# Kernel tuning notes

Hardware: AMD Instinct MI355X
Metric: run time of the kernel (lower is better)

The kernel has to match this reference:

```python
import jax, jax.numpy as jnp
import numpy as np

N, E = 50000, 800000
C = 64
L = 4
EPS_MSG = 1e-7  # GENConv message epsilon


def _bn(h, g, b):
    # BatchNorm over node dim (batch statistics)
    mu = h.mean(0)
    var = h.var(0)
    return (h - mu) * jax.lax.rsqrt(var + 1e-5) * g + b


def _ln(h, g, b):
    mu = h.mean(-1, keepdims=True)
    var = h.var(-1, keepdims=True)
    return (h - mu) * jax.lax.rsqrt(var + 1e-5) * g + b


def _enc(h, W1, b1, g1, B1, W2, b2):
    # PyG MLP(num_layers=2, norm=batch_norm, plain last layer); dropout=identity (eval)
    h = jax.nn.relu(_bn(h @ W1 + b1, g1, B1))
    return h @ W2 + b2


def _genconv(x, e, src, dst, W1, b1, g, B, W2, b2, t):
    n = x.shape[0]
    msg = jax.nn.relu(x[src] + e) + EPS_MSG            # [E, C]
    tm = t * msg
    mx = jax.ops.segment_max(tm, dst, num_segments=n)  # per-dst per-feature max
    w = jnp.exp(tm - mx[dst])
    denom = jax.ops.segment_sum(w, dst, num_segments=n)
    alpha = w / (denom[dst] + 1e-16)                   # scatter softmax weights
    aggr = jax.ops.segment_sum(msg * alpha, dst, num_segments=n)  # [N, C]
    h = aggr + x                                       # GENConv residual
    h = jax.nn.relu(_ln(h @ W1 + b1, g, B))            # inner MLP [C,2C,C]
    return h @ W2 + b2


def _forward(x, edge_attr, src, dst, nW1, nb1, ng1, nB1, nW2, nb2,
             eW1, eb1, eg1, eB1, eW2, eb2, lng, lnb,
             cW1, cb1, cg, cB, cW2, cb2, ct,
             oW1, ob1, og1, oB1, oW2, ob2, og2, oB2, oW3, ob3):
    h = _enc(x, nW1, nb1, ng1, nB1, nW2, nb2)          # [N, C]
    e = _enc(edge_attr, eW1, eb1, eg1, eB1, eW2, eb2)  # [E, C]
    # layers[0].conv applied directly (no pre-norm)
    h = _genconv(h, e, src, dst, cW1[0], cb1[0], cg[0], cB[0], cW2[0], cb2[0], ct[0])
    # DeepGCNLayer res+ : x + conv(relu(LN(x)))
    for l in range(1, L):
        r = jax.nn.relu(_ln(h, lng[l], lnb[l]))
        r = _genconv(r, e, src, dst, cW1[l], cb1[l], cg[l], cB[l], cW2[l], cb2[l], ct[l])
        h = h + r
    # out MLP [C, C//2, C//4, num_classes], batch_norm, plain last
    o = jax.nn.relu(_bn(h @ oW1 + ob1, og1, oB1))
    o = jax.nn.relu(_bn(o @ oW2 + ob2, og2, oB2))
    return o @ oW3 + ob3


def setup_inputs() -> dict:
    key = jax.random.key(0)
    ks = iter(jax.random.split(key, 32))
    def nrm(shape, s=0.05):
        return jax.random.normal(next(ks), shape, dtype=jnp.float32) * s
    inp = {}
    inp["x"] = nrm((N, 16), 1.0)
    inp["edge_attr"] = nrm((E, 8), 1.0)
    inp["edge_index"] = jax.random.randint(next(ks), (2, E), 0, N, dtype=jnp.int32)
    inp["nW1"] = nrm((16, C)); inp["nb1"] = jnp.zeros((C,)); inp["ng1"] = jnp.ones((C,)); inp["nB1"] = jnp.zeros((C,))
    inp["nW2"] = nrm((C, C)); inp["nb2"] = jnp.zeros((C,))
    inp["eW1"] = nrm((8, C)); inp["eb1"] = jnp.zeros((C,)); inp["eg1"] = jnp.ones((C,)); inp["eB1"] = jnp.zeros((C,))
    inp["eW2"] = nrm((C, C)); inp["eb2"] = jnp.zeros((C,))
    inp["lng"] = jnp.ones((L, C)); inp["lnb"] = jnp.zeros((L, C))
    inp["cW1"] = nrm((L, C, 2 * C)); inp["cb1"] = jnp.zeros((L, 2 * C))
    inp["cg"] = jnp.ones((L, 2 * C)); inp["cB"] = jnp.zeros((L, 2 * C))
    inp["cW2"] = nrm((L, 2 * C, C)); inp["cb2"] = jnp.zeros((L, C))
    inp["ct"] = jnp.ones((L,))
    inp["oW1"] = nrm((C, C // 2)); inp["ob1"] = jnp.zeros((C // 2,)); inp["og1"] = jnp.ones((C // 2,)); inp["oB1"] = jnp.zeros((C // 2,))
    inp["oW2"] = nrm((C // 2, C // 4)); inp["ob2"] = jnp.zeros((C // 4,)); inp["og2"] = jnp.ones((C // 4,)); inp["oB2"] = jnp.zeros((C // 4,))
    inp["oW3"] = nrm((C // 4, 2)); inp["ob3"] = jnp.zeros((2,))
    return inp


def reference(x, edge_attr, edge_index, nW1, nb1, ng1, nB1, nW2, nb2,
              eW1, eb1, eg1, eB1, eW2, eb2, lng, lnb,
              cW1, cb1, cg, cB, cW2, cb2, ct,
              oW1, ob1, og1, oB1, oW2, ob2, og2, oB2, oW3, ob3):
    src, dst = edge_index[0], edge_index[1]
    return _forward(x, edge_attr, src, dst, nW1, nb1, ng1, nB1, nW2, nb2,
                    eW1, eb1, eg1, eB1, eW2, eb2, lng, lnb,
                    cW1, cb1, cg, cB, cW2, cb2, ct,
                    oW1, ob1, og1, oB1, oW2, ob2, og2, oB2, oW3, ob3)
```

## Files before the change

### kernel.cpp

```cpp
#include <hip/hip_runtime.h>
#include <cstdint>

#define NN 50000
#define NE 800000

using u16 = unsigned short;
using bf16x8 = __attribute__((ext_vector_type(8))) short;
using f32x4  = __attribute__((ext_vector_type(4))) float;

static constexpr long long OFF_E    = 0;
static constexpr long long OFF_H    = 25600000;
static constexpr long long OFF_R    = 28800000;
static constexpr long long OFF_AG   = 32000000;
static constexpr long long OFF_CSR  = 35200000;
static constexpr long long OFF_ST   = 41600000;
static constexpr size_t    WS_NEED  = (size_t)(OFF_ST + 1024) * 4;

static constexpr long long CSR_ROWPTR = 0;
static constexpr long long CSR_CNT    = 50004;
static constexpr long long CSR_PERM   = 100096;
static constexpr long long CSR_SSRC   = 900096;
static constexpr long long CSR_BSUM   = 1900000;
static constexpr long long CSR_WT     = 2000000;
static constexpr long long CSR_SPART  = 3000000;

__device__ __forceinline__ float bf2f(u16 u){ return __uint_as_float(((unsigned)u) << 16); }
__device__ __forceinline__ u16 f2bf(float f){
    unsigned u = __float_as_uint(f);
    return (u16)((u + 0x7FFFu + ((u >> 16) & 1u)) >> 16);
}

template<int K, bool BF>
__global__ __launch_bounds__(256) void enc1_kernel(
    const float* __restrict__ A, const float* __restrict__ W,
    const float* __restrict__ bias, void* __restrict__ outv,
    const int* __restrict__ permOpt,
    float* __restrict__ stPart, int rows, int tiles)
{
    __shared__ __align__(16) float At[64][K + 4];
    __shared__ __align__(16) float Wl[K][64];
    __shared__ float ssum[64], ssq[64];
    const int tid = threadIdx.x;
    for (int i = tid; i < K * 64; i += 256) Wl[i >> 6][i & 63] = W[i];
    if (tid < 64) { ssum[tid] = 0.f; ssq[tid] = 0.f; }
    const int tx = tid & 15, ty = tid >> 4;
    const float4 bv = *(const float4*)&bias[tx * 4];
    float cs[4] = {0.f,0.f,0.f,0.f}, cq[4] = {0.f,0.f,0.f,0.f};
    constexpr int KC = K / 4;
    __syncthreads();

    for (int tile = blockIdx.x; tile < tiles; tile += gridDim.x){
        const int base = tile * 64;
        for (int i4 = tid; i4 < 64 * KC; i4 += 256){
            int r = i4 / KC, kc = i4 - r * KC;
            int gr = base + r;
            float4 v = {0.f, 0.f, 0.f, 0.f};
            if (gr < rows){
                int orig = permOpt ? permOpt[gr] : gr;
                v = *(const float4*)&A[(long long)orig * K + kc * 4];
            }
            *(float4*)&At[r][kc * 4] = v;
        }
        __syncthreads();
        float acc[4][4];
        #pragma unroll
        for (int i = 0; i < 4; i++){ acc[i][0]=0.f; acc[i][1]=0.f; acc[i][2]=0.f; acc[i][3]=0.f; }
        #pragma unroll
        for (int k4 = 0; k4 < KC; k4++){
            float4 b0 = *(const float4*)&Wl[k4 * 4 + 0][tx * 4];
            float4 b1 = *(const float4*)&Wl[k4 * 4 + 1][tx * 4];
            float4 b2 = *(const float4*)&Wl[k4 * 4 + 2][tx * 4];
            float4 b3 = *(const float4*)&Wl[k4 * 4 + 3][tx * 4];
            #pragma unroll
            for (int i = 0; i < 4; i++){
                float4 a = *(const float4*)&At[ty * 4 + i][k4 * 4];
                acc[i][0] = fmaf(a.x, b0.x, acc[i][0]); acc[i][1] = fmaf(a.x, b0.y, acc[i][1]);
                acc[i][2] = fmaf(a.x, b0.z, acc[i][2]); acc[i][3] = fmaf(a.x, b0.w, acc[i][3]);
                acc[i][0] = fmaf(a.y, b1.x, acc[i][0]); acc[i][1] = fmaf(a.y, b1.y, acc[i][1]);
                acc[i][2] = fmaf(a.y, b1.z, acc[i][2]); acc[i][3] = fmaf(a.y, b1.w, acc[i][3]);
                acc[i][0] = fmaf(a.z, b2.x, acc[i][0]); acc[i][1] = fmaf(a.z, b2.y, acc[i][1]);
                acc[i][2] = fmaf(a.z, b2.z, acc[i][2]); acc[i][3] = fmaf(a.z, b2.w, acc[i][3]);
                acc[i][0] = fmaf(a.w, b3.x, acc[i][0]); acc[i][1] = fmaf(a.w, b3.y, acc[i][1]);
                acc[i][2] = fmaf(a.w, b3.z, acc[i][2]); acc[i][3] = fmaf(a.w, b3.w, acc[i][3]);
            }
        }
        #pragma unroll
        for (int i = 0; i < 4; i++){
            int gr = base + ty * 4 + i;
            if (gr < rows){
                float4 o;
                o.x = acc[i][0] + bv.x; o.y = acc[i][1] + bv.y;
                o.z = acc[i][2] + bv.z; o.w = acc[i][3] + bv.w;
                if (BF){
                    ushort4 s;
                    s.x = f2bf(o.x); s.y = f2bf(o.y); s.z = f2bf(o.z); s.w = f2bf(o.w);
                    *(ushort4*)((u16*)outv + (long long)gr * 64 + tx * 4) = s;
                } else {
                    *(float4*)((float*)outv + (long long)gr * 64 + tx * 4) = o;
                }
                cs[0]+=o.x; cs[1]+=o.y; cs[2]+=o.z; cs[3]+=o.w;
                cq[0]+=o.x*o.x; cq[1]+=o.y*o.y; cq[2]+=o.z*o.z; cq[3]+=o.w*o.w;
            }
        }
        __syncthreads();
    }
    #pragma unroll
    for (int j = 0; j < 4; j++){
        atomicAdd(&ssum[tx * 4 + j], cs[j]);
        atomicAdd(&ssq [tx * 4 + j], cq[j]);
    }
    __syncthreads();
    if (tid < 64){
        stPart[(long long)blockIdx.x * 128 + tid]      = ssum[tid];
        stPart[(long long)blockIdx.x * 128 + 64 + tid] = ssq[tid];
    }
}

__global__ __launch_bounds__(128) void stat_reduce_par(
    const float* __restrict__ part, int nb,
    float* __restrict__ sum, float* __restrict__ sq)
{
    int t = threadIdx.x;
    int b0 = blockIdx.x * 16;
    float s = 0.f;
    #pragma unroll
    for (int j = 0; j < 16; j++){
        int b = b0 + j;
        if (b < nb) s += part[(long long)b * 128 + t];
    }
    if (t < 64) atomicAdd(&sum[t], s);
    else        atomicAdd(&sq[t - 64], s);
}

__global__ void bn_finalize(const float* __restrict__ sum, const float* __restrict__ sq,
                            const float* __restrict__ g, const float* __restrict__ B,
                            float* __restrict__ scale, float* __restrict__ shift,
                            float invCount, int CO)
{
    int t = threadIdx.x;
    if (t < CO){
        float mu = sum[t] * invCount;
        float var = fmaf(-mu, mu, sq[t] * invCount);
        float sc = g[t] * rsqrtf(var + 1e-5f);
        scale[t] = sc;
        shift[t] = fmaf(-mu, sc, B[t]);
    }
}

template<bool BF>
__global__ __launch_bounds__(256) void enc2_kernel(
    void* __restrict__ iov, const float* __restrict__ W, const float* __restrict__ bias,
    const float* __restrict__ scale, const float* __restrict__ shift, int rows)
{
    __shared__ __align__(16) float At[64][68];
    __shared__ __align__(16) float Wl[64][64];
    const int tid = threadIdx.x;
    const int base = blockIdx.x * 64;
    for (int i = tid; i < 4096; i += 256) Wl[i >> 6][i & 63] = W[i];
    for (int i4 = tid; i4 < 1024; i4 += 256){
        int r = i4 >> 4, kc = i4 & 15;
        int gr = base + r;
        float4 v = {0.f, 0.f, 0.f, 0.f};
        if (gr < rows){
            if (BF){
                ushort4 s = *(const ushort4*)((const u16*)iov + (long long)gr * 64 + kc * 4);
                v.x = bf2f(s.x); v.y = bf2f(s.y); v.z = bf2f(s.z); v.w = bf2f(s.w);
            } else {
                v = *(const float4*)((const float*)iov + (long long)gr * 64 + kc * 4);
            }
        }
        float4 o;
        o.x = fmaxf(fmaf(v.x, scale[kc*4+0], shift[kc*4+0]), 0.f);
        o.y = fmaxf(fmaf(v.y, scale[kc*4+1], shift[kc*4+1]), 0.f);
        o.z = fmaxf(fmaf(v.z, scale[kc*4+2], shift[kc*4+2]), 0.f);
        o.w = fmaxf(fmaf(v.w, scale[kc*4+3], shift[kc*4+3]), 0.f);
        *(float4*)&At[r][kc * 4] = o;
    }
    __syncthreads();
    const int tx = tid & 15, ty = tid >> 4;
    float acc[4][4];
    #pragma unroll
    for (int i = 0; i < 4; i++){ acc[i][0]=0.f; acc[i][1]=0.f; acc[i][2]=0.f; acc[i][3]=0.f; }
    #pragma unroll 4
    for (int k4 = 0; k4 < 16; k4++){
        float4 b0 = *(const float4*)&Wl[k4 * 4 + 0][tx * 4];
        float4 b1 = *(const float4*)&Wl[k4 * 4 + 1][tx * 4];
        float4 b2 = *(const float4*)&Wl[k4 * 4 + 2][tx * 4];
        float4 b3 = *(const float4*)&Wl[k4 * 4 + 3][tx * 4];
        #pragma unroll
        for (int i = 0; i < 4; i++){
            float4 a = *(const float4*)&At[ty * 4 + i][k4 * 4];
            acc[i][0] = fmaf(a.x, b0.x, acc[i][0]); acc[i][1] = fmaf(a.x, b0.y, acc[i][1]);
            acc[i][2] = fmaf(a.x, b0.z, acc[i][2]); acc[i][3] = fmaf(a.x, b0.w, acc[i][3]);
            acc[i][0] = fmaf(a.y, b1.x, acc[i][0]); acc[i][1] = fmaf(a.y, b1.y, acc[i][1]);
            acc[i][2] = fmaf(a.y, b1.z, acc[i][2]); acc[i][3] = fmaf(a.y, b1.w, acc[i][3]);
            acc[i][0] = fmaf(a.z, b2.x, acc[i][0]); acc[i][1] = fmaf(a.z, b2.y, acc[i][1]);
            acc[i][2] = fmaf(a.z, b2.z, acc[i][2]); acc[i][3] = fmaf(a.z, b2.w, acc[i][3]);
            acc[i][0] = fmaf(a.w, b3.x, acc[i][0]); acc[i][1] = fmaf(a.w, b3.y, acc[i][1]);
            acc[i][2] = fmaf(a.w, b3.z, acc[i][2]); acc[i][3] = fmaf(a.w, b3.w, acc[i][3]);
        }
    }
    float4 bv = *(const float4*)&bias[tx * 4];
    #pragma unroll
    for (int i = 0; i < 4; i++){
        int gr = base + ty * 4 + i;
        if (gr < rows){
            float4 o;
            o.x = acc[i][0] + bv.x; o.y = acc[i][1] + bv.y;
            o.z = acc[i][2] + bv.z; o.w = acc[i][3] + bv.w;
            if (BF){
                ushort4 s;
                s.x = f2bf(o.x); s.y = f2bf(o.y); s.z = f2bf(o.z); s.w = f2bf(o.w);
                *(ushort4*)((u16*)iov + (long long)gr * 64 + tx * 4) = s;
            } else {
                *(float4*)((float*)iov + (long long)gr * 64 + tx * 4) = o;
            }
        }
    }
}

__global__ void wt_prep_kernel(const float* __restrict__ W, u16* __restrict__ wt)
{
    int i = blockIdx.x * 256 + threadIdx.x;
    if (i < 4096){ int k = i >> 6, c = i & 63; wt[c * 64 + k] = f2bf(W[i]); }
}

__global__ __launch_bounds__(256) void enc2_mfma_kernel(
    u16* __restrict__ e, const u16* __restrict__ wt, const float* __restrict__ bias,
    const float* __restrict__ scale, const float* __restrict__ shift)
{
    __shared__ __align__(16) u16 At[64][72];
    __shared__ __align__(16) u16 Wt[64][72];
    const int tid = threadIdx.x;
    const long long base = (long long)blockIdx.x * 64;
    for (int i = tid; i < 1024; i += 256){
        int c = i >> 4, kc = i & 15;
        *(ushort4*)&Wt[c][kc * 4] = *(const ushort4*)&wt[c * 64 + kc * 4];
    }
    for (int i = tid; i < 1024; i += 256){
        int r = i >> 4, kc = i & 15;
        ushort4 s = *(const ushort4*)&e[(base + r) * 64 + kc * 4];
        float v0 = fmaxf(fmaf(bf2f(s.x), scale[kc*4+0], shift[kc*4+0]), 0.f);
        float v1 = fmaxf(fmaf(bf2f(s.y), scale[kc*4+1], shift[kc*4+1]), 0.f);
        float v2 = fmaxf(fmaf(bf2f(s.z), scale[kc*4+2], shift[kc*4+2]), 0.f);
        float v3 = fmaxf(fmaf(bf2f(s.w), scale[kc*4+3], shift[kc*4+3]), 0.f);
        ushort4 o; o.x = f2bf(v0); o.y = f2bf(v1); o.z = f2bf(v2); o.w = f2bf(v3);
        *(ushort4*)&At[r][kc * 4] = o;
    }
    __syncthreads();
    const int l = tid & 63;
    const int r0 = (tid >> 6) * 16;
    const int lr = l & 15, lk = (l >> 4) * 8;
    f32x4 acc0 = {0.f,0.f,0.f,0.f}, acc1 = {0.f,0.f,0.f,0.f};
    f32x4 acc2 = {0.f,0.f,0.f,0.f}, acc3 = {0.f,0.f,0.f,0.f};
    #pragma unroll
    for (int k0 = 0; k0 < 64; k0 += 32){
        bf16x8 a  = *(const bf16x8*)&At[r0 + lr][k0 + lk];
        bf16x8 b0 = *(const bf16x8*)&Wt[ 0 + lr][k0 + lk];
        bf16x8 b1 = *(const bf16x8*)&Wt[16 + lr][k0 + lk];
        bf16x8 b2 = *(const bf16x8*)&Wt[32 + lr][k0 + lk];
        bf16x8 b3 = *(const bf16x8*)&Wt[48 + lr][k0 + lk];
        acc0 = __builtin_amdgcn_mfma_f32_16x16x32_bf16(a, b0, acc0, 0, 0, 0);
        acc1 = __builtin_amdgcn_mfma_f32_16x16x32_bf16(a, b1, acc1, 0, 0, 0);
        acc2 = __builtin_amdgcn_mfma_f32_16x16x32_bf16(a, b2, acc2, 0, 0, 0);
        acc3 = __builtin_amdgcn_mfma_f32_16x16x32_bf16(a, b3, acc3, 0, 0, 0);
    }
    const int orow = r0 + (l >> 4) * 4;
    const float bb0 = bias[ 0 + lr], bb1 = bias[16 + lr];
    const float bb2 = bias[32 + lr], bb3 = bias[48 + lr];
    #pragma unroll
    for (int r = 0; r < 4; r++){
        long long rb = (base + orow + r) * 64;
        e[rb +  0 + lr] = f2bf(acc0[r] + bb0);
        e[rb + 16 + lr] = f2bf(acc1[r] + bb1);
        e[rb + 32 + lr] = f2bf(acc2[r] + bb2);
        e[rb + 48 + lr] = f2bf(acc3[r] + bb3);
    }
}

__global__ __launch_bounds__(256) void ln_relu_kernel(
    const float* __restrict__ h, float* __restrict__ r,
    const float* __restrict__ g, const float* __restrict__ b, int rows)
{
    int tid = blockIdx.x * 256 + threadIdx.x;
    int row = tid >> 4, fc = tid & 15;
    if (row >= rows) return;
    float4 v = *(const float4*)&h[(long long)row * 64 + fc * 4];
    float s = v.x + v.y + v.z + v.w;
    float q = v.x*v.x + v.y*v.y + v.z*v.z + v.w*v.w;
    #pragma unroll
    for (int m = 1; m < 16; m <<= 1){ s += __shfl_xor(s, m, 64); q += __shfl_xor(q, m, 64); }
    float mu = s * (1.f / 64.f);
    float var = fmaf(-mu, mu, q * (1.f / 64.f));
    float rs = rsqrtf(var + 1e-5f);
    float4 gv = *(const float4*)&g[fc * 4];
    float4 bv = *(const float4*)&b[fc * 4];
    float4 o;
    o.x = fmaxf(fmaf((v.x - mu) * rs, gv.x, bv.x), 0.f);
    o.y = fmaxf(fmaf((v.y - mu) * rs, gv.y, bv.y), 0.f);
    o.z = fmaxf(fmaf((v.z - mu) * rs, gv.z, bv.z), 0.f);
    o.w = fmaxf(fmaf((v.w - mu) * rs, gv.w, bv.w), 0.f);
    *(float4*)&r[(long long)row * 64 + fc * 4] = o;
}

__global__ __launch_bounds__(256) void hist_kernel(
    const int* __restrict__ dst, int* __restrict__ cnt)
{
    int eidx = blockIdx.x * 256 + threadIdx.x;
    if (eidx < NE) atomicAdd(&cnt[dst[eidx]], 1);
}

__global__ __launch_bounds__(1024) void scan1_kernel(
    const int* __restrict__ cnt, int* __restrict__ rowptr, int* __restrict__ bsum, int n)
{
    __shared__ int buf[1024];
    int tid = threadIdx.x;
    int gid = blockIdx.x * 1024 + tid;
    int v = (gid < n) ? cnt[gid] : 0;
    buf[tid] = v;
    __syncthreads();
    for (int off = 1; off < 1024; off <<= 1){
        int add = (tid >= off) ? buf[tid - off] : 0;
        __syncthreads();
        buf[tid] += add;
        __syncthreads();
    }
    if (gid < n) rowptr[gid] = buf[tid] - v;
    if (tid == 1023) bsum[blockIdx.x] = buf[1023];
}

__global__ void scan2_kernel(int* __restrict__ bsum, int B)
{
    int lane = threadIdx.x;
    int v = (lane < B) ? bsum[lane] : 0;
    int orig = v;
    #pragma unroll
    for (int off = 1; off < 64; off <<= 1){
        int u = __shfl_up(v, off, 64);
        if (lane >= off) v += u;
    }
    if (lane < B) bsum[lane] = v - orig;
}

__global__ __launch_bounds__(1024) void scan3_kernel(
    int* __restrict__ rowptr, const int* __restrict__ bsum, int n)
{
    int gid = blockIdx.x * 1024 + threadIdx.x;
    if (gid < n) rowptr[gid] += bsum[blockIdx.x];
    if (gid == 0) rowptr[n] = NE;
}

__global__ __launch_bounds__(256) void scatter_kernel(
    const int* __restrict__ src, const int* __restrict__ dst,
    int* __restrict__ cursor, int* __restrict__ perm, int* __restrict__ ssrc)
{
    int eidx = blockIdx.x * 256 + threadIdx.x;
    if (eidx >= NE) return;
    int pos = atomicAdd(&cursor[dst[eidx]], 1);
    perm[pos] = eidx;
    ssrc[pos] = src[eidx];
}

__global__ __launch_bounds__(256) void aggr_kernel(
    const u16* __restrict__ e, const float* __restrict__ xn,
    const int* __restrict__ ssrc,
    const int* __restrict__ rowptr, float* __restrict__ aggr,
    const float* __restrict__ tptr, int rows)
{
    int node = (blockIdx.x * 256 + threadIdx.x) >> 6;
    int lane = threadIdx.x & 63;
    if (node >= rows) return;
    const float tl = (*tptr) * 1.44269504088896f;
    int beg = rowptr[node], end = rowptr[node + 1];
    float den = 0.f, num = 0.f;
    int i = beg;
    for (; i + 4 <= end; i += 4){
        float ev0 = bf2f(e[(long long)(i + 0) * 64 + lane]);
        float ev1 = bf2f(e[(long long)(i + 1) * 64 + lane]);
        float ev2 = bf2f(e[(long long)(i + 2) * 64 + lane]);
        float ev3 = bf2f(e[(long long)(i + 3) * 64 + lane]);
        int s0 = ssrc[i + 0], s1 = ssrc[i + 1], s2 = ssrc[i + 2], s3 = ssrc[i + 3];
        float xv0 = xn[(long long)s0 * 64 + lane];
        float xv1 = xn[(long long)s1 * 64 + lane];
        float xv2 = xn[(long long)s2 * 64 + lane];
        float xv3 = xn[(long long)s3 * 64 + lane];
        float msg0 = fmaxf(xv0 + ev0, 0.f) + 1e-7f;
        float msg1 = fmaxf(xv1 + ev1, 0.f) + 1e-7f;
        float msg2 = fmaxf(xv2 + ev2, 0.f) + 1e-7f;
        float msg3 = fmaxf(xv3 + ev3, 0.f) + 1e-7f;
        float w0 = exp2f(tl * msg0);
        float w1 = exp2f(tl * msg1);
        float w2 = exp2f(tl * msg2);
        float w3 = exp2f(tl * msg3);
        den += (w0 + w1) + (w2 + w3);
        num += fmaf(msg0, w0, msg1 * w1) + fmaf(msg2, w2, msg3 * w3);
    }
    for (; i < end; ++i){
        float ev = bf2f(e[(long long)i * 64 + lane]);
        int s = ssrc[i];
        float xv = xn[(long long)s * 64 + lane];
        float msg = fmaxf(xv + ev, 0.f) + 1e-7f;
        float w = exp2f(tl * msg);
        den += w;
        num = fmaf(msg, w, num);
    }
    aggr[(long long)node * 64 + lane] = num / (den + 1e-16f);
}

__global__ __launch_bounds__(256) void conv_mlp_kernel(
    const float* __restrict__ rin, const float* __restrict__ aggr,
    float* __restrict__ h,
    const float* __restrict__ W1, const float* __restrict__ b1,
    const float* __restrict__ g, const float* __restrict__ B,
    const float* __restrict__ W2, const float* __restrict__ b2,
    int addToH, int rows)
{
    __shared__ __align__(16) float At[32][68];
    __shared__ __align__(16) float Wl[8192];
    __shared__ __align__(16) float Hs[32][132];
    __shared__ float lred[64];
    __shared__ float lmu[32], lrs[32];
    const int tid = threadIdx.x;
    const int base = blockIdx.x * 32;
    for (int i = tid; i < 8192; i += 256) Wl[i] = W1[i];
    for (int i4 = tid; i4 < 512; i4 += 256){
        int r = i4 >> 4, kc = i4 & 15;
        int gr = base + r;
        float4 v = {0.f, 0.f, 0.f, 0.f};
        if (gr < rows){
            long long idx = (long long)gr * 64 + kc * 4;
            float4 av = *(const float4*)&aggr[idx];
            float4 rv = *(const float4*)&rin[idx];
            v.x = av.x + rv.x; v.y = av.y + rv.y; v.z = av.z + rv.z; v.w = av.w + rv.w;
        }
        *(float4*)&At[r][kc * 4] = v;
    }
    if (tid < 64) lred[tid] = 0.f;
    __syncthreads();
    {
        const int tx = tid & 31, ty = tid >> 5;
        float acc[4][4];
        #pragma unroll
        for (int i = 0; i < 4; i++){ acc[i][0]=0.f; acc[i][1]=0.f; acc[i][2]=0.f; acc[i][3]=0.f; }
        #pragma unroll 4
        for (int k4 = 0; k4 < 16; k4++){
            float4 b0 = *(const float4*)&Wl[(k4 * 4 + 0) * 128 + tx * 4];
            float4 b1 = *(const float4*)&Wl[(k4 * 4 + 1) * 128 + tx * 4];
            float4 b2 = *(const float4*)&Wl[(k4 * 4 + 2) * 128 + tx * 4];
            float4 b3 = *(const float4*)&Wl[(k4 * 4 + 3) * 128 + tx * 4];
            #pragma unroll
            for (int i = 0; i < 4; i++){
                float4 a = *(const float4*)&At[ty * 4 + i][k4 * 4];
                acc[i][0] = fmaf(a.x, b0.x, acc[i][0]); acc[i][1] = fmaf(a.x, b0.y, acc[i][1]);
                acc[i][2] = fmaf(a.x, b0.z, acc[i][2]); acc[i][3] = fmaf(a.x, b0.w, acc[i][3]);
                acc[i][0] = fmaf(a.y, b1.x, acc[i][0]); acc[i][1] = fmaf(a.y, b1.y, acc[i][1]);
                acc[i][2] = fmaf(a.y, b1.z, acc[i][2]); acc[i][3] = fmaf(a.y, b1.w, acc[i][3]);
                acc[i][0] = fmaf(a.z, b2.x, acc[i][0]); acc[i][1] = fmaf(a.z, b2.y, acc[i][1]);
                acc[i][2] = fmaf(a.z, b2.z, acc[i][2]); acc[i][3] = fmaf(a.z, b2.w, acc[i][3]);
                acc[i][0] = fmaf(a.w, b3.x, acc[i][0]); acc[i][1] = fmaf(a.w, b3.y, acc[i][1]);
                acc[i][2] = fmaf(a.w, b3.z, acc[i][2]); acc[i][3] = fmaf(a.w, b3.w, acc[i][3]);
            }
        }
        float4 bv = *(const float4*)&b1[tx * 4];
        #pragma unroll
        for (int i = 0; i < 4; i++){
            float4 o;
            o.x = acc[i][0] + bv.x; o.y = acc[i][1] + bv.y;
            o.z = acc[i][2] + bv.z; o.w = acc[i][3] + bv.w;
            *(float4*)&Hs[ty * 4 + i][tx * 4] = o;
        }
    }
    __syncthreads();
    {
        int row = tid & 31, seg = tid >> 5;
        float s = 0.f, q = 0.f;
        #pragma unroll
        for (int j = 0; j < 16; j++){
            float v = Hs[row][seg * 16 + j];
            s += v; q = fmaf(v, v, q);
        }
        atomicAdd(&lred[row], s);
        atomicAdd(&lred[32 + row], q);
    }
    __syncthreads();
    if (tid < 32){
        float mu = lred[tid] * (1.f / 128.f);
        float var = fmaf(-mu, mu, lred[32 + tid] * (1.f / 128.f));
        lmu[tid] = mu; lrs[tid] = rsqrtf(var + 1e-5f);
    }
    __syncthreads();
    for (int i = tid; i < 4096; i += 256){
        int row = i >> 7, k = i & 127;
        float v = Hs[row][k];
        v = fmaf((v - lmu[row]) * lrs[row], g[k], B[k]);
        Hs[row][k] = fmaxf(v, 0.f);
    }
    __syncthreads();
    for (int i = tid; i < 8192; i += 256) Wl[i] = W2[i];
    __syncthreads();
    {
        const int tx = tid & 15, ty = tid >> 4;
        float acc[2][4];
        #pragma unroll
        for (int i = 0; i < 2; i++){ acc[i][0]=0.f; acc[i][1]=0.f; acc[i][2]=0.f; acc[i][3]=0.f; }
        #pragma unroll 4
        for (int k4 = 0; k4 < 32; k4++){
            float4 b0 = *(const float4*)&Wl[(k4 * 4 + 0) * 64 + tx * 4];
            float4 b1 = *(const float4*)&Wl[(k4 * 4 + 1) * 64 + tx * 4];
            float4 b2 = *(const float4*)&Wl[(k4 * 4 + 2) * 64 + tx * 4];
            float4 b3 = *(const float4*)&Wl[(k4 * 4 + 3) * 64 + tx * 4];
            #pragma unroll
            for (int i = 0; i < 2; i++){
                float4 a = *(const float4*)&Hs[ty * 2 + i][k4 * 4];
                acc[i][0] = fmaf(a.x, b0.x, acc[i][0]); acc[i][1] = fmaf(a.x, b0.y, acc[i][1]);
                acc[i][2] = fmaf(a.x, b0.z, acc[i][2]); acc[i][3] = fmaf(a.x, b0.w, acc[i][3]);
                acc[i][0] = fmaf(a.y, b1.x, acc[i][0]); acc[i][1] = fmaf(a.y, b1.y, acc[i][1]);
                acc[i][2] = fmaf(a.y, b1.z, acc[i][2]); acc[i][3] = fmaf(a.y, b1.w, acc[i][3]);
                acc[i][0] = fmaf(a.z, b2.x, acc[i][0]); acc[i][1] = fmaf(a.z, b2.y, acc[i][1]);
                acc[i][2] = fmaf(a.z, b2.z, acc[i][2]); acc[i][3] = fmaf(a.z, b2.w, acc[i][3]);
                acc[i][0] = fmaf(a.w, b3.x, acc[i][0]); acc[i][1] = fmaf(a.w, b3.y, acc[i][1]);
                acc[i][2] = fmaf(a.w, b3.z, acc[i][2]); acc[i][3] = fmaf(a.w, b3.w, acc[i][3]);
            }
        }
        float4 bv = *(const float4*)&b2[tx * 4];
        #pragma unroll
        for (int i = 0; i < 2; i++){
            int gr = base + ty * 2 + i;
            if (gr < rows){
                float4 o;
                o.x = acc[i][0] + bv.x; o.y = acc[i][1] + bv.y;
                o.z = acc[i][2] + bv.z; o.w = acc[i][3] + bv.w;
                long long idx = (long long)gr * 64 + tx * 4;
                if (addToH){
                    float4 c = *(const float4*)&h[idx];
                    o.x += c.x; o.y += c.y; o.z += c.z; o.w += c.w;
                }
                *(float4*)&h[idx] = o;
            }
        }
    }
}

__global__ __launch_bounds__(256) void out1_kernel(
    const float* __restrict__ A, const float* __restrict__ W, const float* __restrict__ bias,
    float* __restrict__ out, float* __restrict__ stSum, float* __restrict__ stSq, int rows)
{
    __shared__ __align__(16) float At[64][68];
    __shared__ __align__(16) float Wl[64][32];
    __shared__ float ssum[32], ssq[32];
    const int tid = threadIdx.x;
    const int base = blockIdx.x * 64;
    for (int i = tid; i < 2048; i += 256) Wl[i >> 5][i & 31] = W[i];
    if (tid < 32){ ssum[tid] = 0.f; ssq[tid] = 0.f; }
    for (int i4 = tid; i4 < 1024; i4 += 256){
        int r = i4 >> 4, kc = i4 & 15;
        int gr = base + r;
        float4 v = {0.f, 0.f, 0.f, 0.f};
        if (gr < rows) v = *(const float4*)&A[(long long)gr * 64 + kc * 4];
        *(float4*)&At[r][kc * 4] = v;
    }
    __syncthreads();
    const int row = tid >> 2, lane = tid & 3;
    const int gr = base + row;
    float acc[8];
    #pragma unroll
    for (int j = 0; j < 8; j++) acc[j] = bias[lane * 8 + j];
    #pragma unroll 4
    for (int k4 = 0; k4 < 16; k4++){
        float4 a = *(const float4*)&At[row][k4 * 4];
        float av[4] = {a.x, a.y, a.z, a.w};
        #pragma unroll
        for (int j = 0; j < 4; j++){
            float4 w0 = *(const float4*)&Wl[k4 * 4 + j][lane * 8];
            float4 w1 = *(const float4*)&Wl[k4 * 4 + j][lane * 8 + 4];
            acc[0] = fmaf(av[j], w0.x, acc[0]); acc[1] = fmaf(av[j], w0.y, acc[1]);
            acc[2] = fmaf(av[j], w0.z, acc[2]); acc[3] = fmaf(av[j], w0.w, acc[3]);
            acc[4] = fmaf(av[j], w1.x, acc[4]); acc[5] = fmaf(av[j], w1.y, acc[5]);
            acc[6] = fmaf(av[j], w1.z, acc[6]); acc[7] = fmaf(av[j], w1.w, acc[7]);
        }
    }
    if (gr < rows){
        float4 o0 = {acc[0], acc[1], acc[2], acc[3]};
        float4 o1 = {acc[4], acc[5], acc[6], acc[7]};
        *(float4*)&out[(long long)gr * 32 + lane * 8]     = o0;
        *(float4*)&out[(long long)gr * 32 + lane * 8 + 4] = o1;
        #pragma unroll
        for (int j = 0; j < 8; j++){
            atomicAdd(&ssum[lane * 8 + j], acc[j]);
            atomicAdd(&ssq [lane * 8 + j], acc[j] * acc[j]);
        }
    }
    __syncthreads();
    if (tid < 32){ atomicAdd(&stSum[tid], ssum[tid]); atomicAdd(&stSq[tid], ssq[tid]); }
}

__global__ __launch_bounds__(256) void out2_kernel(
    const float* __restrict__ A, const float* __restrict__ W, const float* __restrict__ bias,
    float* __restrict__ out, const float* __restrict__ sc, const float* __restrict__ sh,
    float* __restrict__ stSum, float* __restrict__ stSq, int rows)
{
    __shared__ __align__(16) float At[64][36];
    __shared__ __align__(16) float Wl[32][16];
    __shared__ float ssum[16], ssq[16];
    const int tid = threadIdx.x;
    const int base = blockIdx.x * 64;
    for (int i = tid; i < 512; i += 256) Wl[i >> 4][i & 15] = W[i];
    if (tid < 16){ ssum[tid] = 0.f; ssq[tid] = 0.f; }
    for (int i4 = tid; i4 < 512; i4 += 256){
        int r = i4 >> 3, kc = i4 & 7;
        int gr = base + r;
        float4 v = {0.f, 0.f, 0.f, 0.f};
        if (gr < rows) v = *(const float4*)&A[(long long)gr * 32 + kc * 4];
        float4 o;
        o.x = fmaxf(fmaf(v.x, sc[kc*4+0], sh[kc*4+0]), 0.f);
        o.y = fmaxf(fmaf(v.y, sc[kc*4+1], sh[kc*4+1]), 0.f);
        o.z = fmaxf(fmaf(v.z, sc[kc*4+2], sh[kc*4+2]), 0.f);
        o.w = fmaxf(fmaf(v.w, sc[kc*4+3], sh[kc*4+3]), 0.f);
        *(float4*)&At[r][kc * 4] = o;
    }
    __syncthreads();
    const int row = tid >> 2, lane = tid & 3;
    const int gr = base + row;
    float acc[4];
    #pragma unroll
    for (int j = 0; j < 4; j++) acc[j] = bias[lane * 4 + j];
    #pragma unroll 2
    for (int k4 = 0; k4 < 8; k4++){
        float4 a = *(const float4*)&At[row][k4 * 4];
        float av[4] = {a.x, a.y, a.z, a.w};
        #pragma unroll
        for (int j = 0; j < 4; j++){
            float4 w = *(const float4*)&Wl[k4 * 4 + j][lane * 4];
            acc[0] = fmaf(av[j], w.x, acc[0]); acc[1] = fmaf(av[j], w.y, acc[1]);
            acc[2] = fmaf(av[j], w.z, acc[2]); acc[3] = fmaf(av[j], w.w, acc[3]);
        }
    }
    if (gr < rows){
        float4 o = {acc[0], acc[1], acc[2], acc[3]};
        *(float4*)&out[(long long)gr * 16 + lane * 4] = o;
        #pragma unroll
        for (int j = 0; j < 4; j++){
            atomicAdd(&ssum[lane * 4 + j], acc[j]);
            atomicAdd(&ssq [lane * 4 + j], acc[j] * acc[j]);
        }
    }
    __syncthreads();
    if (tid < 16){ atomicAdd(&stSum[tid], ssum[tid]); atomicAdd(&stSq[tid], ssq[tid]); }
}

__global__ __launch_bounds__(256) void out3_kernel(
    const float* __restrict__ A, const float* __restrict__ W, const float* __restrict__ bias,
    const float* __restrict__ sc, const float* __restrict__ sh,
    float* __restrict__ out, int rows)
{
    int row = blockIdx.x * 256 + threadIdx.x;
    if (row >= rows) return;
    float o0 = bias[0], o1 = bias[1];
    #pragma unroll
    for (int k = 0; k < 16; k++){
        float a = fmaxf(fmaf(A[(long long)row * 16 + k], sc[k], sh[k]), 0.f);
        o0 = fmaf(a, W[k * 2 + 0], o0);
        o1 = fmaf(a, W[k * 2 + 1], o1);
    }
    out[(long long)row * 2 + 0] = o0;
    out[(long long)row * 2 + 1] = o1;
}

extern "C" void kernel_launch(void* const* d_in, const int* in_sizes, int n_in,
                              void* d_out, int out_size, void* d_ws, size_t ws_size,
                              hipStream_t stream)
{
    (void)in_sizes; (void)n_in; (void)out_size;
    if (ws_size < WS_NEED) return;

    const float* x    = (const float*)d_in[0];
    const float* ea   = (const float*)d_in[1];
    const int*   eidx = (const int*)  d_in[2];
    const float* nW1  = (const float*)d_in[3];
    const float* nb1  = (const float*)d_in[4];
    const float* ng1  = (const float*)d_in[5];
    const float* nB1  = (const float*)d_in[6];
    const float* nW2  = (const float*)d_in[7];
    const float* nb2  = (const float*)d_in[8];
    const float* eW1  = (const float*)d_in[9];
    const float* eb1  = (const float*)d_in[10];
    const float* eg1  = (const float*)d_in[11];
    const float* eB1  = (const float*)d_in[12];
    const float* eW2  = (const float*)d_in[13];
    const float* eb2  = (const float*)d_in[14];
    const float* lng  = (const float*)d_in[15];
    const float* lnb  = (const float*)d_in[16];
    const float* cW1  = (const float*)d_in[17];
    const float* cb1  = (const float*)d_in[18];
    const float* cg   = (const float*)d_in[19];
    const float* cB   = (const float*)d_in[20];
    const float* cW2  = (const float*)d_in[21];
    const float* cb2  = (const float*)d_in[22];
    const float* ct   = (const float*)d_in[23];
    const float* oW1  = (const float*)d_in[24];
    const float* ob1  = (const float*)d_in[25];
    const float* og1  = (const float*)d_in[26];
    const float* oB1  = (const float*)d_in[27];
    const float* oW2  = (const float*)d_in[28];
    const float* ob2  = (const float*)d_in[29];
    const float* og2  = (const float*)d_in[30];
    const float* oB2  = (const float*)d_in[31];
    const float* oW3  = (const float*)d_in[32];
    const float* ob3  = (const float*)d_in[33];

    float* ws = (float*)d_ws;
    u16*   e    = (u16*)(ws + OFF_E);
    float* h    = ws + OFF_H;
    float* r    = ws + OFF_R;
    float* aggr = ws + OFF_AG;
    int*   csr  = (int*)(ws + OFF_CSR);
    int*   rowptr = csr + CSR_ROWPTR;
    int*   cnt    = csr + CSR_CNT;
    int*   perm   = csr + CSR_PERM;
    int*   ssrc   = csr + CSR_SSRC;
    int*   bsum   = csr + CSR_BSUM;
    u16*   wt     = (u16*)(csr + CSR_WT);
    float* stPart = (float*)(csr + CSR_SPART);
    float* t1   = ws + OFF_AG;
    float* t2   = ws + OFF_AG + 1600000;
    float* st   = ws + OFF_ST;
    float* sumA = st;        float* sqA = st + 128;
    float* scA  = st + 256;  float* shA = st + 384;
    float* sumB = st + 512;  float* sqB = st + 640;
    float* scB  = st + 768;  float* shB = st + 896;

    const int* src = eidx;
    const int* dst = eidx + NE;
    const int SCAN_B = (NN + 1023) / 1024;

    (void)hipMemsetAsync(cnt, 0, NN * sizeof(int), stream);
    hist_kernel<<<(NE + 255) / 256, 256, 0, stream>>>(dst, cnt);
    scan1_kernel<<<SCAN_B, 1024, 0, stream>>>(cnt, rowptr, bsum, NN);
    scan2_kernel<<<1, 64, 0, stream>>>(bsum, SCAN_B);
    scan3_kernel<<<SCAN_B, 1024, 0, stream>>>(rowptr, bsum, NN);
    (void)hipMemcpyAsync(cnt, rowptr, NN * sizeof(int), hipMemcpyDeviceToDevice, stream);
    scatter_kernel<<<(NE + 255) / 256, 256, 0, stream>>>(src, dst, cnt, perm, ssrc);
    wt_prep_kernel<<<16, 256, 0, stream>>>(eW2, wt);

    (void)hipMemsetAsync(st, 0, 256 * sizeof(float), stream);
    enc1_kernel<16, false><<<1024, 256, 0, stream>>>(x, nW1, nb1, h, nullptr, stPart, NN, (NN + 63) / 64);
    stat_reduce_par<<<64, 128, 0, stream>>>(stPart, 1024, sumA, sqA);
    bn_finalize<<<1, 128, 0, stream>>>(sumA, sqA, ng1, nB1, scA, shA, 1.f / NN, 64);
    enc2_kernel<false><<<(NN + 63) / 64, 256, 0, stream>>>(h, nW2, nb2, scA, shA, NN);
    (void)hipMemsetAsync(st, 0, 256 * sizeof(float), stream);
    enc1_kernel<8, true><<<2048, 256, 0, stream>>>(ea, eW1, eb1, e, perm, stPart, NE, NE / 64);
    stat_reduce_par<<<128, 128, 0, stream>>>(stPart, 2048, sumA, sqA);
    bn_finalize<<<1, 128, 0, stream>>>(sumA, sqA, eg1, eB1, scA, shA, 1.f / NE, 64);
    enc2_mfma_kernel<<<NE / 64, 256, 0, stream>>>(e, wt, eb2, scA, shA);

    for (int l = 0; l < 4; l++){
        const float* rin = (l == 0) ? h : r;
        if (l > 0)
            ln_relu_kernel<<<(NN * 16) / 256, 256, 0, stream>>>(h, r, lng + l * 64, lnb + l * 64, NN);
        aggr_kernel<<<(NN * 64 + 255) / 256, 256, 0, stream>>>(
            e, rin, ssrc, rowptr, aggr, ct + l, NN);
        conv_mlp_kernel<<<(NN + 31) / 32, 256, 0, stream>>>(
            rin, aggr, h,
            cW1 + (long long)l * 8192, cb1 + l * 128, cg + l * 128, cB + l * 128,
            cW2 + (long long)l * 8192, cb2 + l * 64, (l > 0) ? 1 : 0, NN);
    }

    (void)hipMemsetAsync(st, 0, 1024 * sizeof(float), stream);
    out1_kernel<<<(NN + 63) / 64, 256, 0, stream>>>(h, oW1, ob1, t1, sumA, sqA, NN);
    bn_finalize<<<1, 128, 0, stream>>>(sumA, sqA, og1, oB1, scA, shA, 1.f / NN, 32);
    out2_kernel<<<(NN + 63) / 64, 256, 0, stream>>>(t1, oW2, ob2, t2, scA, shA, sumB, sqB, NN);
    bn_finalize<<<1, 128, 0, stream>>>(sumB, sqB, og2, oB2, scB, shB, 1.f / NN, 16);
    out3_kernel<<<(NN + 255) / 256, 256, 0, stream>>>(t2, oW3, ob3, scB, shB, (float*)d_out, NN);
}
```

Before: 697.9 us.

## Use bf16 MFMA for the GENConv inner MLP with pre-transposed weights

Replaces the fp32 FMA-based two-layer conv MLP with a bf16 MFMA version that processes 64 rows per block. The weights are converted once into transposed bf16 buffers by a new prep kernel. The LayerNorm intermediate is held in bf16 shared memory, and the W2 tile reuses the first GEMM's shared buffer. This targets ALU time and LDS footprint in the per-layer MLP, at the cost of bf16 rounding of activations and the intermediate, plus scalar stores of the final output.

```diff
diff --git a/kernel.cpp b/kernel.cpp
--- a/kernel.cpp
+++ b/kernel.cpp
@@ -22,6 +22,8 @@
 static constexpr long long CSR_SSRC   = 900096;
 static constexpr long long CSR_BSUM   = 1900000;
 static constexpr long long CSR_WT     = 2000000;
+static constexpr long long CSR_WT1    = 2100000;
+static constexpr long long CSR_WT2    = 2200000;
 static constexpr long long CSR_SPART  = 3000000;
 
 __device__ __forceinline__ float bf2f(u16 u){ return __uint_as_float(((unsigned)u) << 16); }
@@ -223,6 +225,22 @@
 {
     int i = blockIdx.x * 256 + threadIdx.x;
     if (i < 4096){ int k = i >> 6, c = i & 63; wt[c * 64 + k] = f2bf(W[i]); }
+}
+
+__global__ void cw_prep_kernel(const float* __restrict__ cW1, const float* __restrict__ cW2,
+                               u16* __restrict__ wt1, u16* __restrict__ wt2)
+{
+    int i = blockIdx.x * 256 + threadIdx.x;
+    if (i < 32768){
+        int l = i >> 13, j = i & 8191;
+        int c = j >> 6, k = j & 63;
+        wt1[(long long)l * 8192 + c * 64 + k] = f2bf(cW1[(long long)l * 8192 + k * 128 + c]);
+    } else if (i < 65536){
+        int t = i - 32768;
+        int l = t >> 13, j = t & 8191;
+        int c = j >> 7, k = j & 127;
+        wt2[(long long)l * 8192 + c * 128 + k] = f2bf(cW2[(long long)l * 8192 + k * 64 + c]);
+    }
 }
 
 __global__ __launch_bounds__(256) void enc2_mfma_kernel(
@@ -407,23 +425,25 @@
     aggr[(long long)node * 64 + lane] = num / (den + 1e-16f);
 }
 
-__global__ __launch_bounds__(256) void conv_mlp_kernel(
+__global__ __launch_bounds__(256) void conv_mlp_mfma_kernel(
     const float* __restrict__ rin, const float* __restrict__ aggr,
     float* __restrict__ h,
-    const float* __restrict__ W1, const float* __restrict__ b1,
+    const u16* __restrict__ w1g, const float* __restrict__ b1,
     const float* __restrict__ g, const float* __restrict__ B,
-    const float* __restrict__ W2, const float* __restrict__ b2,
+    const u16* __restrict__ w2g, const float* __restrict__ b2,
     int addToH, int rows)
 {
-    __shared__ __align__(16) float At[32][68];
-    __shared__ __align__(16) float Wl[8192];
-    __shared__ __align__(16) float Hs[32][132];
-    __shared__ float lred[64];
-    __shared__ float lmu[32], lrs[32];
+    __shared__ __align__(16) u16 poolA[64 * 72 + 128 * 72];
+    __shared__ __align__(16) u16 Hsb[64][136];
+    __shared__ float lred[128];
+    __shared__ float lmu[64], lrs[64];
+    u16 (*At)[72]   = (u16(*)[72])poolA;
+    u16 (*W1t)[72]  = (u16(*)[72])(poolA + 64 * 72);
+    u16 (*W2t)[136] = (u16(*)[136])poolA;
+
     const int tid = threadIdx.x;
-    const int base = blockIdx.x * 32;
-    for (int i = tid; i < 8192; i += 256) Wl[i] = W1[i];
-    for (int i4 = tid; i4 < 512; i4 += 256){
+    const int base = blockIdx.x * 64;
+    for (int i4 = tid; i4 < 1024; i4 += 256){
         int r = i4 >> 4, kc = i4 & 15;
         int gr = base + r;
         float4 v = {0.f, 0.f, 0.f, 0.f};
@@ -433,109 +453,115 @@
             float4 rv = *(const float4*)&rin[idx];
             v.x = av.x + rv.x; v.y = av.y + rv.y; v.z = av.z + rv.z; v.w = av.w + rv.w;
         }
-        *(float4*)&At[r][kc * 4] = v;
-    }
-    if (tid < 64) lred[tid] = 0.f;
-    __syncthreads();
+        ushort4 o; o.x = f2bf(v.x); o.y = f2bf(v.y); o.z = f2bf(v.z); o.w = f2bf(v.w);
+        *(ushort4*)&At[r][kc * 4] = o;
+    }
+    for (int i4 = tid; i4 < 2048; i4 += 256){
+        int c = i4 >> 4, kc = i4 & 15;
+        *(ushort4*)&W1t[c][kc * 4] = *(const ushort4*)&w1g[c * 64 + kc * 4];
+    }
+    if (tid < 128) lred[tid] = 0.f;
+    __syncthreads();
+
+    const int l = tid & 63;
+    const int r0 = (tid >> 6) * 16;
+    const int lr = l & 15, lk = (l >> 4) * 8;
+    const int orow = r0 + (l >> 4) * 4;
+
     {
-        const int tx = tid & 31, ty = tid >> 5;
-        float acc[4][4];
-        #pragma unroll
-        for (int i = 0; i < 4; i++){ acc[i][0]=0.f; acc[i][1]=0.f; acc[i][2]=0.f; acc[i][3]=0.f; }
-        #pragma unroll 4
-        for (int k4 = 0; k4 < 16; k4++){
-            float4 b0 = *(const float4*)&Wl[(k4 * 4 + 0) * 128 + tx * 4];
-            float4 b1 = *(const float4*)&Wl[(k4 * 4 + 1) * 128 + tx * 4];
-            float4 b2 = *(const float4*)&Wl[(k4 * 4 + 2) * 128 + tx * 4];
-            float4 b3 = *(const float4*)&Wl[(k4 * 4 + 3) * 128 + tx * 4];
+        f32x4 acc[8];
+        #pragma unroll
+        for (int ct = 0; ct < 8; ct++) acc[ct] = (f32x4){0.f,0.f,0.f,0.f};
+        #pragma unroll
+        for (int k0 = 0; k0 < 64; k0 += 32){
+            bf16x8 a = *(const bf16x8*)&At[r0 + lr][k0 + lk];
             #pragma unroll
-            for (int i = 0; i < 4; i++){
-                float4 a = *(const float4*)&At[ty * 4 + i][k4 * 4];
-                acc[i][0] = fmaf(a.x, b0.x, acc[i][0]); acc[i][1] = fmaf(a.x, b0.y, acc[i][1]);
-                acc[i][2] = fmaf(a.x, b0.z, acc[i][2]); acc[i][3] = fmaf(a.x, b0.w, acc[i][3]);
-                acc[i][0] = fmaf(a.y, b1.x, acc[i][0]); acc[i][1] = fmaf(a.y, b1.y, acc[i][1]);
-                acc[i][2] = fmaf(a.y, b1.z, acc[i][2]); acc[i][3] = fmaf(a.y, b1.w, acc[i][3]);
-                acc[i][0] = fmaf(a.z, b2.x, acc[i][0]); acc[i][1] = fmaf(a.z, b2.y, acc[i][1]);
-                acc[i][2] = fmaf(a.z, b2.z, acc[i][2]); acc[i][3] = fmaf(a.z, b2.w, acc[i][3]);
-                acc[i][0] = fmaf(a.w, b3.x, acc[i][0]); acc[i][1] = fmaf(a.w, b3.y, acc[i][1]);
-                acc[i][2] = fmaf(a.w, b3.z, acc[i][2]); acc[i][3] = fmaf(a.w, b3.w, acc[i][3]);
+            for (int ct = 0; ct < 8; ct++){
+                bf16x8 b = *(const bf16x8*)&W1t[ct * 16 + lr][k0 + lk];
+                acc[ct] = __builtin_amdgcn_mfma_f32_16x16x32_bf16(a, b, acc[ct], 0, 0, 0);
             }
         }
-        float4 bv = *(const float4*)&b1[tx * 4];
-        #pragma unroll
-        for (int i = 0; i < 4; i++){
-            float4 o;
-            o.x = acc[i][0] + bv.x; o.y = acc[i][1] + bv.y;
-            o.z = acc[i][2] + bv.z; o.w = acc[i][3] + bv.w;
-            *(float4*)&Hs[ty * 4 + i][tx * 4] = o;
-        }
-    }
-    __syncthreads();
+        #pragma unroll
+        for (int ct = 0; ct < 8; ct++){
+            int col = ct * 16 + lr;
+            float bb = b1[col];
+            #pragma unroll
+            for (int r = 0; r < 4; r++)
+                Hsb[orow + r][col] = f2bf(acc[ct][r] + bb);
+        }
+    }
+    __syncthreads();
+
     {
-        int row = tid & 31, seg = tid >> 5;
+        int row = tid & 63, seg = tid >> 6;
         float s = 0.f, q = 0.f;
         #pragma unroll
-        for (int j = 0; j < 16; j++){
-            float v = Hs[row][seg * 16 + j];
-            s += v; q = fmaf(v, v, q);
+        for (int j4 = 0; j4 < 8; j4++){
+            ushort4 hv = *(const ushort4*)&Hsb[row][seg * 32 + j4 * 4];
+            float v0 = bf2f(hv.x), v1 = bf2f(hv.y), v2 = bf2f(hv.z), v3 = bf2f(hv.w);
+            s += (v0 + v1) + (v2 + v3);
+            q += fmaf(v0, v0, v1 * v1) + fmaf(v2, v2, v3 * v3);
         }
         atomicAdd(&lred[row], s);
-        atomicAdd(&lred[32 + row], q);
-    }
-    __syncthreads();
-    if (tid < 32){
+        atomicAdd(&lred[64 + row], q);
+        for (int i4 = tid; i4 < 2048; i4 += 256){
+            int c = i4 >> 5, kc = i4 & 31;
+            *(ushort4*)&W2t[c][kc * 4] = *(const ushort4*)&w2g[c * 128 + kc * 4];
+        }
+    }
+    __syncthreads();
+    if (tid < 64){
         float mu = lred[tid] * (1.f / 128.f);
-        float var = fmaf(-mu, mu, lred[32 + tid] * (1.f / 128.f));
+        float var = fmaf(-mu, mu, lred[64 + tid] * (1.f / 128.f));
         lmu[tid] = mu; lrs[tid] = rsqrtf(var + 1e-5f);
     }
     __syncthreads();
-    for (int i = tid; i < 4096; i += 256){
-        int row = i >> 7, k = i & 127;
-        float v = Hs[row][k];
-        v = fmaf((v - lmu[row]) * lrs[row], g[k], B[k]);
-        Hs[row][k] = fmaxf(v, 0.f);
-    }
-    __syncthreads();
-    for (int i = tid; i < 8192; i += 256) Wl[i] = W2[i];
-    __syncthreads();
+
     {
-        const int tx = tid & 15, ty = tid >> 4;
-        float acc[2][4];
-        #pragma unroll
-        for (int i = 0; i < 2; i++){ acc[i][0]=0.f; acc[i][1]=0.f; acc[i][2]=0.f; acc[i][3]=0.f; }
-        #pragma unroll 4
-        for (int k4 = 0; k4 < 32; k4++){
-            float4 b0 = *(const float4*)&Wl[(k4 * 4 + 0) * 64 + tx * 4];
-            float4 b1 = *(const float4*)&Wl[(k4 * 4 + 1) * 64 + tx * 4];
-            float4 b2 = *(const float4*)&Wl[(k4 * 4 + 2) * 64 + tx * 4];
-            float4 b3 = *(const float4*)&Wl[(k4 * 4 + 3) * 64 + tx * 4];
+        int row = tid & 63, seg = tid >> 6;
+        float mu = lmu[row], rs = lrs[row];
+        #pragma unroll
+        for (int j4 = 0; j4 < 8; j4++){
+            int k = seg * 32 + j4 * 4;
+            ushort4 hv = *(const ushort4*)&Hsb[row][k];
+            float4 gv = *(const float4*)&g[k];
+            float4 Bv = *(const float4*)&B[k];
+            float v0 = fmaxf(fmaf((bf2f(hv.x) - mu) * rs, gv.x, Bv.x), 0.f);
+            float v1 = fmaxf(fmaf((bf2f(hv.y) - mu) * rs, gv.y, Bv.y), 0.f);
+            float v2 = fmaxf(fmaf((bf2f(hv.z) - mu) * rs, gv.z, Bv.z), 0.f);
+            float v3 = fmaxf(fmaf((bf2f(hv.w) - mu) * rs, gv.w, Bv.w), 0.f);
+            ushort4 o; o.x = f2bf(v0); o.y = f2bf(v1); o.z = f2bf(v2); o.w = f2bf(v3);
+            *(ushort4*)&Hsb[row][k] = o;
+        }
+    }
+    __syncthreads();
+
+    {
+        f32x4 acc[4];
+        #pragma unroll
+        for (int ct = 0; ct < 4; ct++) acc[ct] = (f32x4){0.f,0.f,0.f,0.f};
+        #pragma unroll
+        for (int k0 = 0; k0 < 128; k0 += 32){
+            bf16x8 a = *(const bf16x8*)&Hsb[r0 + lr][k0 + lk];
             #pragma unroll
-            for (int i = 0; i < 2; i++){
-                float4 a = *(const float4*)&Hs[ty * 2 + i][k4 * 4];
-                acc[i][0] = fmaf(a.x, b0.x, acc[i][0]); acc[i][1] = fmaf(a.x, b0.y, acc[i][1]);
-                acc[i][2] = fmaf(a.x, b0.z, acc[i][2]); acc[i][3] = fmaf(a.x, b0.w, acc[i][3]);
-                acc[i][0] = fmaf(a.y, b1.x, acc[i][0]); acc[i][1] = fmaf(a.y, b1.y, acc[i][1]);
-                acc[i][2] = fmaf(a.y, b1.z, acc[i][2]); acc[i][3] = fmaf(a.y, b1.w, acc[i][3]);
-                acc[i][0] = fmaf(a.z, b2.x, acc[i][0]); acc[i][1] = fmaf(a.z, b2.y, acc[i][1]);
-                acc[i][2] = fmaf(a.z, b2.z, acc[i][2]); acc[i][3] = fmaf(a.z, b2.w, acc[i][3]);
-                acc[i][0] = fmaf(a.w, b3.x, acc[i][0]); acc[i][1] = fmaf(a.w, b3.y, acc[i][1]);
-                acc[i][2] = fmaf(a.w, b3.z, acc[i][2]); acc[i][3] = fmaf(a.w, b3.w, acc[i][3]);
+            for (int ct = 0; ct < 4; ct++){
+                bf16x8 b = *(const bf16x8*)&W2t[ct * 16 + lr][k0 + lk];
+                acc[ct] = __builtin_amdgcn_mfma_f32_16x16x32_bf16(a, b, acc[ct], 0, 0, 0);
             }
         }
-        float4 bv = *(const float4*)&b2[tx * 4];
-        #pragma unroll
-        for (int i = 0; i < 2; i++){
-            int gr = base + ty * 2 + i;
-            if (gr < rows){
-                float4 o;
-                o.x = acc[i][0] + bv.x; o.y = acc[i][1] + bv.y;
-                o.z = acc[i][2] + bv.z; o.w = acc[i][3] + bv.w;
-                long long idx = (long long)gr * 64 + tx * 4;
-                if (addToH){
-                    float4 c = *(const float4*)&h[idx];
-                    o.x += c.x; o.y += c.y; o.z += c.z; o.w += c.w;
+        #pragma unroll
+        for (int ct = 0; ct < 4; ct++){
+            int col = ct * 16 + lr;
+            float bb = b2[col];
+            #pragma unroll
+            for (int r = 0; r < 4; r++){
+                int gr = base + orow + r;
+                if (gr < rows){
+                    long long idx = (long long)gr * 64 + col;
+                    float v = acc[ct][r] + bb;
+                    if (addToH) v += h[idx];
+                    h[idx] = v;
                 }
-                *(float4*)&h[idx] = o;
             }
         }
     }
@@ -720,6 +746,8 @@
     int*   ssrc   = csr + CSR_SSRC;
     int*   bsum   = csr + CSR_BSUM;
     u16*   wt     = (u16*)(csr + CSR_WT);
+    u16*   wt1    = (u16*)(csr + CSR_WT1);
+    u16*   wt2    = (u16*)(csr + CSR_WT2);
     float* stPart = (float*)(csr + CSR_SPART);
     float* t1   = ws + OFF_AG;
     float* t2   = ws + OFF_AG + 1600000;
@@ -741,6 +769,7 @@
     (void)hipMemcpyAsync(cnt, rowptr, NN * sizeof(int), hipMemcpyDeviceToDevice, stream);
     scatter_kernel<<<(NE + 255) / 256, 256, 0, stream>>>(src, dst, cnt, perm, ssrc);
     wt_prep_kernel<<<16, 256, 0, stream>>>(eW2, wt);
+    cw_prep_kernel<<<256, 256, 0, stream>>>(cW1, cW2, wt1, wt2);
 
     (void)hipMemsetAsync(st, 0, 256 * sizeof(float), stream);
     enc1_kernel<16, false><<<1024, 256, 0, stream>>>(x, nW1, nb1, h, nullptr, stPart, NN, (NN + 63) / 64);
@@ -759,10 +788,10 @@
             ln_relu_kernel<<<(NN * 16) / 256, 256, 0, stream>>>(h, r, lng + l * 64, lnb + l * 64, NN);
         aggr_kernel<<<(NN * 64 + 255) / 256, 256, 0, stream>>>(
             e, rin, ssrc, rowptr, aggr, ct + l, NN);
-        conv_mlp_kernel<<<(NN + 31) / 32, 256, 0, stream>>>(
+        conv_mlp_mfma_kernel<<<(NN + 63) / 64, 256, 0, stream>>>(
             rin, aggr, h,
-            cW1 + (long long)l * 8192, cb1 + l * 128, cg + l * 128, cB + l * 128,
-            cW2 + (long long)l * 8192, cb2 + l * 64, (l > 0) ? 1 : 0, NN);
+            wt1 + (long long)l * 8192, cb1 + l * 128, cg + l * 128, cB + l * 128,
+            wt2 + (long long)l * 8192, cb2 + l * 64, (l > 0) ? 1 : 0, NN);
     }
 
     (void)hipMemsetAsync(st, 0, 1024 * sizeof(float), stream);
```

Measured after the change: 622.9 us. 10.7% less time.
